# Kernel optimization log

Measured on AMD Instinct MI355X. Metric: run time of the kernel, lower is better.

Reference implementation:

```python
import jax, jax.numpy as jnp
import numpy as np

E = 1024  # embed_dim
R = 16    # LoRA rank
B = 4
S = 2048


def setup_inputs() -> dict:
    key = jax.random.key(0)
    ks = jax.random.split(key, 12)
    inp = {
        'query': jax.random.normal(ks[0], (B, S, E), jnp.float32),
        'key': jax.random.normal(ks[1], (B, S, E), jnp.float32),
        'value': jax.random.normal(ks[2], (B, S, E), jnp.float32),
        'Q_weight': jax.random.normal(ks[3], (E, E), jnp.float32) / np.sqrt(E),
        'K_weight': jax.random.normal(ks[4], (E, E), jnp.float32) / np.sqrt(E),
        'V_weight': jax.random.normal(ks[5], (E, E), jnp.float32) / np.sqrt(E),
        'Q_A': 0.02 * jax.random.normal(ks[6], (R, E), jnp.float32),
        'Q_B': 0.02 * jax.random.normal(ks[7], (E, R), jnp.float32),
        'K_A': 0.02 * jax.random.normal(ks[8], (R, E), jnp.float32),
        'K_B': 0.02 * jax.random.normal(ks[9], (E, R), jnp.float32),
        'V_A': 0.02 * jax.random.normal(ks[10], (R, E), jnp.float32),
        'V_B': 0.02 * jax.random.normal(ks[11], (E, R), jnp.float32),
        'O_weight': jax.random.normal(jax.random.fold_in(key, 99), (E, E), jnp.float32) / np.sqrt(E),
    }
    return inp


def reference(query, key, value, Q_weight, K_weight, V_weight,
              Q_A, Q_B, K_A, K_B, V_A, V_B, O_weight):
    embed_dim = Q_weight.shape[0]
    # base projections (linear(x, W) = x @ W.T) + low-rank LoRA deltas
    Q = jnp.einsum('bse,fe->bsf', query, Q_weight) + jnp.einsum('bse,re->bsr', query, Q_A) @ Q_B.T
    K = jnp.einsum('bse,fe->bsf', key, K_weight) + jnp.einsum('bse,re->bsr', key, K_A) @ K_B.T
    V = jnp.einsum('bse,fe->bsf', value, V_weight) + jnp.einsum('bse,re->bsr', value, V_A) @ V_B.T
    scores = jnp.einsum('bqe,bke->bqk', Q, K) / jnp.sqrt(jnp.float32(embed_dim))
    attn = jax.nn.softmax(scores, axis=-1)
    out = jnp.einsum('bqk,bke->bqe', attn, V)
    return jnp.einsum('bse,fe->bsf', out, O_weight)
```

## Files before the change

kernel.cpp:

```cpp
#include <hip/hip_runtime.h>


#define S_LEN 2048
#define E_DIM 1024

typedef __attribute__((ext_vector_type(8))) short short8;
typedef __attribute__((ext_vector_type(4))) float floatx4;

__device__ __forceinline__ unsigned short f2bf(float f) {
  union { float f; unsigned int u; } x; x.f = f;
  return (unsigned short)((x.u + 0x7fffu + ((x.u >> 16) & 1u)) >> 16);
}
__device__ __forceinline__ float bf2f(unsigned short h) {
  union { unsigned int u; float f; } x; x.u = ((unsigned int)h) << 16;
  return x.f;
}

__device__ __forceinline__ void gld_lds16(const unsigned short* g, unsigned short* l) {
  __builtin_amdgcn_global_load_lds(
      (const __attribute__((address_space(1))) unsigned int*)(const void*)g,
      (__attribute__((address_space(3))) unsigned int*)(void*)l,
      16, 0, 0);
}

template<bool LORA, bool OUTF32, bool OWNM>
__global__ __launch_bounds__(512, 2) void gemm256(
    const unsigned short* __restrict__ A, const unsigned short* __restrict__ B,
    void* __restrict__ Cv,
    const unsigned short* __restrict__ LA, const unsigned short* __restrict__ LB,
    long lda, long ldb, long ldc, int K, float scale,
    long batA, long batB, long batC, long batLA, long batLB) {
  __shared__ alignas(16) unsigned short As[2][2][8192];
  __shared__ alignas(16) unsigned short Bs[2][2][8192];

  const int tid  = threadIdx.x;
  const int wave = tid >> 6, lane = tid & 63;
  const int quad = lane >> 4, l16 = lane & 15;
  const int wr = wave >> 2, wc = wave & 3;
  const int bg = (wc & 1) * 4;

  const int Nx = (int)gridDim.x, Ny = (int)gridDim.y;
  const int wg2 = (int)blockIdx.x + Nx * (int)blockIdx.y;
  const int xcd = wg2 & 7, ii = wg2 >> 3;
  int bx, by;
  if constexpr (OWNM) {
    const int lg = 31 - __clz(Nx);
    by = xcd * (Ny >> 3) + (ii >> lg);
    bx = ii & (Nx - 1);
  } else {
    const int lg = 31 - __clz(Ny);
    bx = xcd * (Nx >> 3) + (ii >> lg);
    by = ii & (Ny - 1);
  }
  const long m0 = (long)by * 256;
  const long n0 = (long)bx * 256;
  const unsigned short* Az = A + (long)blockIdx.z * batA;
  const unsigned short* Bz = B + (long)blockIdx.z * batB;

  floatx4 acc[8][4];
#pragma unroll
  for (int i = 0; i < 8; ++i)
#pragma unroll
    for (int j = 0; j < 4; ++j) acc[i][j] = (floatx4){0.f, 0.f, 0.f, 0.f};

  const int c0r = ((tid >> 7) << 4) | (tid & 15);
  const int c0k = ((tid >> 4) & 7) << 3;
  const unsigned short* a0 = Az + (m0 + c0r) * lda + c0k;
  const unsigned short* b0 = Bz + (n0 + c0r) * ldb + c0k;

#define STG_A(bf, h, k0)                                                    \
  do {                                                                      \
    gld_lds16(a0 + (long)((h) * 128) * lda + (k0), &As[bf][h][tid * 8]);    \
    gld_lds16(a0 + (long)((h) * 128 + 64) * lda + (k0),                     \
              &As[bf][h][4096 + tid * 8]);                                  \
  } while (0)
#define STG_B(bf, h, k0)                                                    \
  do {                                                                      \
    gld_lds16(b0 + (long)((h) * 128) * ldb + (k0), &Bs[bf][h][tid * 8]);    \
    gld_lds16(b0 + (long)((h) * 128 + 64) * ldb + (k0),                     \
              &Bs[bf][h][4096 + tid * 8]);                                  \
  } while (0)

  STG_A(0, 0, 0); STG_A(0, 1, 0);
  STG_B(0, 0, 0); STG_B(0, 1, 0);
  STG_A(1, 0, 64); STG_A(1, 1, 64);

  const int NT = K >> 6;
#pragma unroll 2
  for (int t = 0; t < NT; ++t) {
    const int cur = t & 1;
    const int kB = (t + 1 < NT ? t + 1 : NT - 1) << 6;
    const int kA = (t + 2 < NT ? t + 2 : NT - 1) << 6;
    const unsigned short* ra = &As[cur][wr][0];
    const unsigned short* rb = &Bs[cur][wc >> 1][0];

    asm volatile("s_waitcnt vmcnt(4)\n\ts_barrier" ::: "memory");

    short8 a_[8][2], b_[4][2];
#pragma unroll
    for (int i = 0; i < 4; ++i)
#pragma unroll
      for (int ks = 0; ks < 2; ++ks)
        a_[i][ks] = *(const short8*)(ra + (i * 128 + ks * 64 + lane) * 8);
#pragma unroll
    for (int j = 0; j < 2; ++j)
#pragma unroll
      for (int ks = 0; ks < 2; ++ks)
        b_[j][ks] = *(const short8*)(rb + ((bg + j) * 128 + ks * 64 + lane) * 8);
    STG_B(cur ^ 1, 0, kB);
    asm volatile("s_barrier" ::: "memory");
    __builtin_amdgcn_s_setprio(1);
#pragma unroll
    for (int ks = 0; ks < 2; ++ks)
#pragma unroll
      for (int i = 0; i < 4; ++i)
#pragma unroll
        for (int j = 0; j < 2; ++j)
          acc[i][j] = __builtin_amdgcn_mfma_f32_16x16x32_bf16(a_[i][ks], b_[j][ks], acc[i][j], 0, 0, 0);
    __builtin_amdgcn_s_setprio(0);

#pragma unroll
    for (int i = 4; i < 8; ++i)
#pragma unroll
      for (int ks = 0; ks < 2; ++ks)
        a_[i][ks] = *(const short8*)(ra + (i * 128 + ks * 64 + lane) * 8);
#pragma unroll
    for (int j = 2; j < 4; ++j)
#pragma unroll
      for (int ks = 0; ks < 2; ++ks)
        b_[j][ks] = *(const short8*)(rb + ((bg + j) * 128 + ks * 64 + lane) * 8);
    STG_B(cur ^ 1, 1, kB);
    asm volatile("s_barrier" ::: "memory");
    __builtin_amdgcn_s_setprio(1);
#pragma unroll
    for (int ks = 0; ks < 2; ++ks)
#pragma unroll
      for (int i = 0; i < 4; ++i)
#pragma unroll
        for (int j = 2; j < 4; ++j)
          acc[i][j] = __builtin_amdgcn_mfma_f32_16x16x32_bf16(a_[i][ks], b_[j][ks], acc[i][j], 0, 0, 0);
    __builtin_amdgcn_s_setprio(0);
    asm volatile("s_waitcnt lgkmcnt(0)\n\ts_barrier" ::: "memory");

    STG_A(cur, 0, kA);
    __builtin_amdgcn_s_setprio(1);
#pragma unroll
    for (int ks = 0; ks < 2; ++ks)
#pragma unroll
      for (int i = 4; i < 8; ++i)
#pragma unroll
        for (int j = 0; j < 2; ++j)
          acc[i][j] = __builtin_amdgcn_mfma_f32_16x16x32_bf16(a_[i][ks], b_[j][ks], acc[i][j], 0, 0, 0);
    __builtin_amdgcn_s_setprio(0);

    STG_A(cur, 1, kA);
    __builtin_amdgcn_s_setprio(1);
#pragma unroll
    for (int ks = 0; ks < 2; ++ks)
#pragma unroll
      for (int i = 4; i < 8; ++i)
#pragma unroll
        for (int j = 2; j < 4; ++j)
          acc[i][j] = __builtin_amdgcn_mfma_f32_16x16x32_bf16(a_[i][ks], b_[j][ks], acc[i][j], 0, 0, 0);
    __builtin_amdgcn_s_setprio(0);
  }

  if constexpr (LORA) {
    __syncthreads();
    const unsigned short* LAz = LA + (long)blockIdx.z * batLA;
    const unsigned short* LBz = LB + (long)blockIdx.z * batLB;
#pragma unroll
    for (int cc = 0; cc < 4; ++cc) {
      const int c = cc * 512 + tid;
      const int h = c >> 10, ci = c & 1023;
      const int kc = (ci >> 4) & 7;
      const int row = h * 128 + ((ci >> 7) << 4) + (ci & 15);
      uint4 va, vb_;
      if (kc < 2) {
        va  = *(const uint4*)(LAz + (m0 + row) * 16 + kc * 8);
        vb_ = *(const uint4*)(LBz + (n0 + row) * 16 + kc * 8);
      } else {
        va.x = va.y = va.z = va.w = 0u; vb_ = va;
      }
      *(uint4*)(&As[0][h][ci * 8]) = va;
      *(uint4*)(&Bs[0][h][ci * 8]) = vb_;
    }
    __syncthreads();
    short8 a2[8], b2[4];
#pragma unroll
    for (int i = 0; i < 8; ++i)
      a2[i] = *(const short8*)(&As[0][wr][(i * 128 + lane) * 8]);
#pragma unroll
    for (int j = 0; j < 4; ++j)
      b2[j] = *(const short8*)(&Bs[0][wc >> 1][((bg + j) * 128 + lane) * 8]);
#pragma unroll
    for (int i = 0; i < 8; ++i)
#pragma unroll
      for (int j = 0; j < 4; ++j)
        acc[i][j] = __builtin_amdgcn_mfma_f32_16x16x32_bf16(a2[i], b2[j], acc[i][j], 0, 0, 0);
  } else {
    asm volatile("s_waitcnt vmcnt(0)" ::: "memory");
  }

#pragma unroll
  for (int i = 0; i < 8; ++i) {
    const long row = m0 + wr * 128 + i * 16 + quad * 4;
#pragma unroll
    for (int j = 0; j < 4; ++j) {
      const long col = n0 + wc * 64 + j * 16 + l16;
#pragma unroll
      for (int rr = 0; rr < 4; ++rr) {
        float val = acc[i][j][rr] * scale;
        if constexpr (OUTF32)
          ((float*)Cv)[(long)blockIdx.z * batC + (row + rr) * ldc + col] = val;
        else
          ((unsigned short*)Cv)[(long)blockIdx.z * batC + (row + rr) * ldc + col] = f2bf(val);
      }
    }
  }
#undef STG_A
#undef STG_B
}

__device__ __forceinline__ uint4 pack8(const float* x) {
  float4 a = *(const float4*)x;
  float4 b = *(const float4*)(x + 4);
  uint4 o;
  o.x = (unsigned int)f2bf(a.x) | ((unsigned int)f2bf(a.y) << 16);
  o.y = (unsigned int)f2bf(a.z) | ((unsigned int)f2bf(a.w) << 16);
  o.z = (unsigned int)f2bf(b.x) | ((unsigned int)f2bf(b.y) << 16);
  o.w = (unsigned int)f2bf(b.z) | ((unsigned int)f2bf(b.w) << 16);
  return o;
}

__global__ __launch_bounds__(256) void prep_qkv(
    const float* __restrict__ q, const float* __restrict__ k, const float* __restrict__ v,
    unsigned short* __restrict__ qb, unsigned short* __restrict__ kb,
    unsigned short* __restrict__ vb) {
  const float* X; unsigned short* Y;
  if (blockIdx.y == 0)      { X = q; Y = qb; }
  else if (blockIdx.y == 1) { X = k; Y = kb; }
  else                      { X = v; Y = vb; }
  const int tid = threadIdx.x;
  const long blk = (long)blockIdx.x * 16384;
#pragma unroll
  for (int it = 0; it < 8; ++it) {
    const long idx = blk + it * 2048 + tid * 8;
    *(uint4*)(Y + idx) = pack8(X + idx);
  }
}

__global__ __launch_bounds__(256) void cvt_all(
    const float* __restrict__ Wq, const float* __restrict__ Wk,
    const float* __restrict__ Wv, const float* __restrict__ Wo,
    const float* __restrict__ QB, const float* __restrict__ KB, const float* __restrict__ VB,
    const float* __restrict__ QA, const float* __restrict__ KA, const float* __restrict__ VA,
    unsigned short* __restrict__ wqb, unsigned short* __restrict__ wkb,
    unsigned short* __restrict__ wvb, unsigned short* __restrict__ wob,
    unsigned short* __restrict__ Bqb, unsigned short* __restrict__ Bkb, unsigned short* __restrict__ Bvb,
    unsigned short* __restrict__ Aqb, unsigned short* __restrict__ Akb, unsigned short* __restrict__ Avb) {
  if (blockIdx.y < 4) {
    const float* x; unsigned short* y;
    switch (blockIdx.y) {
      case 0: x = Wq; y = wqb; break;
      case 1: x = Wk; y = wkb; break;
      case 2: x = Wv; y = wvb; break;
      default: x = Wo; y = wob; break;
    }
    const long i = ((long)blockIdx.x * 256 + threadIdx.x) * 8;
    *(uint4*)(y + i) = pack8(x + i);
  } else {
    if (blockIdx.x >= 48) return;
    const int mat = blockIdx.x >> 3, sub = blockIdx.x & 7;
    const float* x; unsigned short* y;
    switch (mat) {
      case 0: x = QB; y = Bqb; break;
      case 1: x = KB; y = Bkb; break;
      case 2: x = VB; y = Bvb; break;
      case 3: x = QA; y = Aqb; break;
      case 4: x = KA; y = Akb; break;
      default: x = VA; y = Avb; break;
    }
    const long i = ((long)sub * 256 + threadIdx.x) * 8;
    *(uint4*)(y + i) = pack8(x + i);
  }
}

__global__ __launch_bounds__(256) void lora_t_mfma(
    const unsigned short* __restrict__ qb, const unsigned short* __restrict__ kb,
    const unsigned short* __restrict__ vb,
    const unsigned short* __restrict__ Aq, const unsigned short* __restrict__ Ak,
    const unsigned short* __restrict__ Av,
    unsigned short* __restrict__ Tq, unsigned short* __restrict__ Tk,
    unsigned short* __restrict__ Tv) {
  const unsigned short* X; const unsigned short* Am; unsigned short* T;
  if (blockIdx.y == 0)      { X = qb; Am = Aq; T = Tq; }
  else if (blockIdx.y == 1) { X = kb; Am = Ak; T = Tk; }
  else                      { X = vb; Am = Av; T = Tv; }
  const int tid = threadIdx.x, wave = tid >> 6, lane = tid & 63;
  const int quad = lane >> 4, l16 = lane & 15;
  const long m0 = (long)blockIdx.x * 64 + wave * 16;
  floatx4 acc = (floatx4){0.f, 0.f, 0.f, 0.f};
  const unsigned short* xp = X + (m0 + l16) * 1024 + quad * 8;
  const unsigned short* ap = Am + (long)l16 * 1024 + quad * 8;
#pragma unroll 4
  for (int k0 = 0; k0 < 1024; k0 += 32) {
    short8 af = *(const short8*)(xp + k0);
    short8 bf = *(const short8*)(ap + k0);
    acc = __builtin_amdgcn_mfma_f32_16x16x32_bf16(af, bf, acc, 0, 0, 0);
  }
#pragma unroll
  for (int rr = 0; rr < 4; ++rr)
    T[(m0 + quad * 4 + rr) * 16 + l16] = f2bf(acc[rr]);
}

__global__ __launch_bounds__(256) void softmax_kernel(unsigned short* __restrict__ S) {
  const long base = (long)blockIdx.x * 2048;
  const int tid = threadIdx.x;
  const int lane = tid & 63, wave = tid >> 6;
  __shared__ float redm[4], reds[4];
  uint4 raw = *(const uint4*)(S + base + tid * 8);
  unsigned int w[4] = {raw.x, raw.y, raw.z, raw.w};
  float v[8];
#pragma unroll
  for (int i = 0; i < 4; ++i) {
    v[2 * i]     = bf2f((unsigned short)(w[i] & 0xffffu));
    v[2 * i + 1] = bf2f((unsigned short)(w[i] >> 16));
  }
  float m = v[0];
#pragma unroll
  for (int i = 1; i < 8; ++i) m = fmaxf(m, v[i]);
  for (int off = 32; off >= 1; off >>= 1) m = fmaxf(m, __shfl_xor(m, off, 64));
  if (lane == 0) redm[wave] = m;
  __syncthreads();
  m = fmaxf(fmaxf(redm[0], redm[1]), fmaxf(redm[2], redm[3]));
  float e[8], s = 0.f;
#pragma unroll
  for (int i = 0; i < 8; ++i) { e[i] = __expf(v[i] - m); s += e[i]; }
  for (int off = 32; off >= 1; off >>= 1) s += __shfl_xor(s, off, 64);
  if (lane == 0) reds[wave] = s;
  __syncthreads();
  s = reds[0] + reds[1] + reds[2] + reds[3];
  const float inv = 1.0f / s;
  uint4 o;
  o.x = (unsigned int)f2bf(e[0] * inv) | ((unsigned int)f2bf(e[1] * inv) << 16);
  o.y = (unsigned int)f2bf(e[2] * inv) | ((unsigned int)f2bf(e[3] * inv) << 16);
  o.z = (unsigned int)f2bf(e[4] * inv) | ((unsigned int)f2bf(e[5] * inv) << 16);
  o.w = (unsigned int)f2bf(e[6] * inv) | ((unsigned int)f2bf(e[7] * inv) << 16);
  *(uint4*)(S + base + tid * 8) = o;
}

extern "C" void kernel_launch(void* const* d_in, const int* in_sizes, int n_in,
                              void* d_out, int out_size, void* d_ws, size_t ws_size,
                              hipStream_t stream) {
  const float* q  = (const float*)d_in[0];
  const float* k  = (const float*)d_in[1];
  const float* v  = (const float*)d_in[2];
  const float* Wq = (const float*)d_in[3];
  const float* Wk = (const float*)d_in[4];
  const float* Wv = (const float*)d_in[5];
  const float* QA = (const float*)d_in[6];
  const float* QB = (const float*)d_in[7];
  const float* KA = (const float*)d_in[8];
  const float* KB = (const float*)d_in[9];
  const float* VA = (const float*)d_in[10];
  const float* VB = (const float*)d_in[11];
  const float* Wo = (const float*)d_in[12];

  unsigned short* W = (unsigned short*)d_ws;
  const long SEe = (long)8192 * 1024;
  unsigned short* qb  = W;
  unsigned short* kb  = W + SEe;
  unsigned short* vb  = W + 2 * SEe;
  unsigned short* Qp  = W + 3 * SEe;
  unsigned short* Kp  = W + 4 * SEe;
  unsigned short* VT  = W + 5 * SEe;
  unsigned short* wqb = W + 6 * SEe;
  unsigned short* wkb = wqb + 1048576;
  unsigned short* wvb = wkb + 1048576;
  unsigned short* wob = wvb + 1048576;
  unsigned short* Bqb = wob + 1048576;
  unsigned short* Bkb = Bqb + 16384;
  unsigned short* Bvb = Bkb + 16384;
  unsigned short* Aqb = Bvb + 16384;
  unsigned short* Akb = Aqb + 16384;
  unsigned short* Avb = Akb + 16384;
  unsigned short* Tq  = Avb + 16384;
  unsigned short* Tk  = Tq + 131072;
  unsigned short* Tv  = Tk + 131072;
  unsigned short* scores = W;
  unsigned short* attn   = vb;

  dim3 blk(256, 1, 1), blk5(512, 1, 1);
  prep_qkv<<<dim3(512, 3, 1), blk, 0, stream>>>(q, k, v, qb, kb, vb);
  cvt_all<<<dim3(512, 5, 1), blk, 0, stream>>>(Wq, Wk, Wv, Wo, QB, KB, VB, QA, KA, VA,
                                               wqb, wkb, wvb, wob, Bqb, Bkb, Bvb, Aqb, Akb, Avb);
  lora_t_mfma<<<dim3(128, 3, 1), blk, 0, stream>>>(qb, kb, vb, Aqb, Akb, Avb, Tq, Tk, Tv);

  gemm256<true, false, true><<<dim3(4, 32, 2), blk5, 0, stream>>>(
      qb, wqb, Qp, Tq, Bqb, 1024, 1024, 1024, 1024, 1.0f,
      SEe, 1048576, SEe, 131072, 16384);
  gemm256<true, false, false><<<dim3(32, 4, 1), blk5, 0, stream>>>(
      wvb, vb, VT, Bvb, Tv, 1024, 1024, 8192, 1024, 1.0f, 0, 0, 0, 0, 0);
  gemm256<false, false, true><<<dim3(8, 8, 4), blk5, 0, stream>>>(
      Qp, Kp, scores, nullptr, nullptr, 1024, 1024, 2048, 1024, 0.03125f,
      (long)S_LEN * E_DIM, (long)S_LEN * E_DIM, (long)S_LEN * S_LEN, 0, 0);
  softmax_kernel<<<8192, blk, 0, stream>>>(scores);
  gemm256<false, false, true><<<dim3(4, 8, 4), blk5, 0, stream>>>(
      scores, VT, attn, nullptr, nullptr, 2048, 8192, 1024, 2048, 1.0f,
      (long)S_LEN * S_LEN, (long)S_LEN, (long)S_LEN * E_DIM, 0, 0);
  gemm256<false, true, true><<<dim3(4, 32, 1), blk5, 0, stream>>>(
      attn, wob, d_out, nullptr, nullptr, 1024, 1024, 1024, 1024, 1.0f, 0, 0, 0, 0, 0);
}
```

Baseline: 432.5 us.

## Template GEMM N-tile width and use 256x128 tiles for smaller GEMMs

Adds a BN template parameter so the GEMM can run with 256x128 output tiles, halving the B-tile LDS footprint and accumulator count, and uses it for the V projection, attn@V and output projection. This doubles block counts for those launches (128->256 or 256->512 blocks), filling more of the CUs. The main loop is also restructured to load per-k-step fragments (aLo/aHi, bb) with extra barriers instead of holding both k-substeps in registers, cutting register pressure but adding synchronisation and reducing A-tile reuse per block.

```diff
diff --git a/kernel.cpp b/kernel.cpp
--- a/kernel.cpp
+++ b/kernel.cpp
@@ -23,21 +23,24 @@
       16, 0, 0);
 }
 
-template<bool LORA, bool OUTF32, bool OWNM>
+template<bool LORA, bool OUTF32, bool OWNM, int BN>
 __global__ __launch_bounds__(512, 2) void gemm256(
     const unsigned short* __restrict__ A, const unsigned short* __restrict__ B,
     void* __restrict__ Cv,
     const unsigned short* __restrict__ LA, const unsigned short* __restrict__ LB,
     long lda, long ldb, long ldc, int K, float scale,
     long batA, long batB, long batC, long batLA, long batLB) {
+  constexpr int BNH = BN / 2;
+  constexpr int BCH = BNH * 8;
+  constexpr int JW  = BN / 64;
   __shared__ alignas(16) unsigned short As[2][2][8192];
-  __shared__ alignas(16) unsigned short Bs[2][2][8192];
+  __shared__ alignas(16) unsigned short Bs[2][2][BCH * 8];
 
   const int tid  = threadIdx.x;
   const int wave = tid >> 6, lane = tid & 63;
   const int quad = lane >> 4, l16 = lane & 15;
   const int wr = wave >> 2, wc = wave & 3;
-  const int bg = (wc & 1) * 4;
+  const int bg = (wc & 1) * JW;
 
   const int Nx = (int)gridDim.x, Ny = (int)gridDim.y;
   const int wg2 = (int)blockIdx.x + Nx * (int)blockIdx.y;
@@ -53,15 +56,15 @@
     by = ii & (Ny - 1);
   }
   const long m0 = (long)by * 256;
-  const long n0 = (long)bx * 256;
+  const long n0 = (long)bx * BN;
   const unsigned short* Az = A + (long)blockIdx.z * batA;
   const unsigned short* Bz = B + (long)blockIdx.z * batB;
 
-  floatx4 acc[8][4];
+  floatx4 acc[8][JW];
 #pragma unroll
   for (int i = 0; i < 8; ++i)
 #pragma unroll
-    for (int j = 0; j < 4; ++j) acc[i][j] = (floatx4){0.f, 0.f, 0.f, 0.f};
+    for (int j = 0; j < JW; ++j) acc[i][j] = (floatx4){0.f, 0.f, 0.f, 0.f};
 
   const int c0r = ((tid >> 7) << 4) | (tid & 15);
   const int c0k = ((tid >> 4) & 7) << 3;
@@ -76,9 +79,10 @@
   } while (0)
 #define STG_B(bf, h, k0)                                                    \
   do {                                                                      \
-    gld_lds16(b0 + (long)((h) * 128) * ldb + (k0), &Bs[bf][h][tid * 8]);    \
-    gld_lds16(b0 + (long)((h) * 128 + 64) * ldb + (k0),                     \
-              &Bs[bf][h][4096 + tid * 8]);                                  \
+    gld_lds16(b0 + (long)((h) * BNH) * ldb + (k0), &Bs[bf][h][tid * 8]);    \
+    if constexpr (BN == 256)                                                \
+      gld_lds16(b0 + (long)((h) * BNH + 64) * ldb + (k0),                   \
+                &Bs[bf][h][4096 + tid * 8]);                                \
   } while (0)
 
   STG_A(0, 0, 0); STG_A(0, 1, 0);
@@ -96,76 +100,73 @@
 
     asm volatile("s_waitcnt vmcnt(4)\n\ts_barrier" ::: "memory");
 
-    short8 a_[8][2], b_[4][2];
-#pragma unroll
-    for (int i = 0; i < 4; ++i)
-#pragma unroll
-      for (int ks = 0; ks < 2; ++ks)
-        a_[i][ks] = *(const short8*)(ra + (i * 128 + ks * 64 + lane) * 8);
-#pragma unroll
-    for (int j = 0; j < 2; ++j)
-#pragma unroll
-      for (int ks = 0; ks < 2; ++ks)
-        b_[j][ks] = *(const short8*)(rb + ((bg + j) * 128 + ks * 64 + lane) * 8);
+    short8 aLo[4], aHi[4], bb[JW];
+#pragma unroll
+    for (int i = 0; i < 4; ++i)
+      aLo[i] = *(const short8*)(ra + (i * 128 + lane) * 8);
+#pragma unroll
+    for (int j = 0; j < JW; ++j)
+      bb[j] = *(const short8*)(rb + ((bg + j) * 128 + lane) * 8);
     STG_B(cur ^ 1, 0, kB);
     asm volatile("s_barrier" ::: "memory");
     __builtin_amdgcn_s_setprio(1);
 #pragma unroll
-    for (int ks = 0; ks < 2; ++ks)
-#pragma unroll
-      for (int i = 0; i < 4; ++i)
-#pragma unroll
-        for (int j = 0; j < 2; ++j)
-          acc[i][j] = __builtin_amdgcn_mfma_f32_16x16x32_bf16(a_[i][ks], b_[j][ks], acc[i][j], 0, 0, 0);
+    for (int i = 0; i < 4; ++i)
+#pragma unroll
+      for (int j = 0; j < JW; ++j)
+        acc[i][j] = __builtin_amdgcn_mfma_f32_16x16x32_bf16(aLo[i], bb[j], acc[i][j], 0, 0, 0);
     __builtin_amdgcn_s_setprio(0);
-
-#pragma unroll
-    for (int i = 4; i < 8; ++i)
-#pragma unroll
-      for (int ks = 0; ks < 2; ++ks)
-        a_[i][ks] = *(const short8*)(ra + (i * 128 + ks * 64 + lane) * 8);
-#pragma unroll
-    for (int j = 2; j < 4; ++j)
-#pragma unroll
-      for (int ks = 0; ks < 2; ++ks)
-        b_[j][ks] = *(const short8*)(rb + ((bg + j) * 128 + ks * 64 + lane) * 8);
+    asm volatile("s_barrier" ::: "memory");
+
+#pragma unroll
+    for (int i = 0; i < 4; ++i)
+      aHi[i] = *(const short8*)(ra + ((i + 4) * 128 + lane) * 8);
     STG_B(cur ^ 1, 1, kB);
     asm volatile("s_barrier" ::: "memory");
     __builtin_amdgcn_s_setprio(1);
 #pragma unroll
-    for (int ks = 0; ks < 2; ++ks)
-#pragma unroll
-      for (int i = 0; i < 4; ++i)
-#pragma unroll
-        for (int j = 2; j < 4; ++j)
-          acc[i][j] = __builtin_amdgcn_mfma_f32_16x16x32_bf16(a_[i][ks], b_[j][ks], acc[i][j], 0, 0, 0);
+    for (int i = 0; i < 4; ++i)
+#pragma unroll
+      for (int j = 0; j < JW; ++j)
+        acc[i + 4][j] = __builtin_amdgcn_mfma_f32_16x16x32_bf16(aHi[i], bb[j], acc[i + 4][j], 0, 0, 0);
     __builtin_amdgcn_s_setprio(0);
+    asm volatile("s_barrier" ::: "memory");
+
+#pragma unroll
+    for (int i = 0; i < 4; ++i)
+      aLo[i] = *(const short8*)(ra + (i * 128 + 64 + lane) * 8);
+#pragma unroll
+    for (int j = 0; j < JW; ++j)
+      bb[j] = *(const short8*)(rb + ((bg + j) * 128 + 64 + lane) * 8);
+    asm volatile("s_barrier" ::: "memory");
+    __builtin_amdgcn_s_setprio(1);
+#pragma unroll
+    for (int i = 0; i < 4; ++i)
+#pragma unroll
+      for (int j = 0; j < JW; ++j)
+        acc[i][j] = __builtin_amdgcn_mfma_f32_16x16x32_bf16(aLo[i], bb[j], acc[i][j], 0, 0, 0);
+    __builtin_amdgcn_s_setprio(0);
+    asm volatile("s_barrier" ::: "memory");
+
+#pragma unroll
+    for (int i = 0; i < 4; ++i)
+      aHi[i] = *(const short8*)(ra + ((i + 4) * 128 + 64 + lane) * 8);
+    asm volatile("s_barrier" ::: "memory");
+    __builtin_amdgcn_s_setprio(1);
+#pragma unroll
+    for (int i = 0; i < 4; ++i)
+#pragma unroll
+      for (int j = 0; j < JW; ++j)
+        acc[i + 4][j] = __builtin_amdgcn_mfma_f32_16x16x32_bf16(aHi[i], bb[j], acc[i + 4][j], 0, 0, 0);
+    __builtin_amdgcn_s_setprio(0);
+
     asm volatile("s_waitcnt lgkmcnt(0)\n\ts_barrier" ::: "memory");
-
     STG_A(cur, 0, kA);
-    __builtin_amdgcn_s_setprio(1);
-#pragma unroll
-    for (int ks = 0; ks < 2; ++ks)
-#pragma unroll
-      for (int i = 4; i < 8; ++i)
-#pragma unroll
-        for (int j = 0; j < 2; ++j)
-          acc[i][j] = __builtin_amdgcn_mfma_f32_16x16x32_bf16(a_[i][ks], b_[j][ks], acc[i][j], 0, 0, 0);
-    __builtin_amdgcn_s_setprio(0);
-
     STG_A(cur, 1, kA);
-    __builtin_amdgcn_s_setprio(1);
-#pragma unroll
-    for (int ks = 0; ks < 2; ++ks)
-#pragma unroll
-      for (int i = 4; i < 8; ++i)
-#pragma unroll
-        for (int j = 2; j < 4; ++j)
-          acc[i][j] = __builtin_amdgcn_mfma_f32_16x16x32_bf16(a_[i][ks], b_[j][ks], acc[i][j], 0, 0, 0);
-    __builtin_amdgcn_s_setprio(0);
   }
 
   if constexpr (LORA) {
+    asm volatile("s_waitcnt vmcnt(0)" ::: "memory");
     __syncthreads();
     const unsigned short* LAz = LA + (long)blockIdx.z * batLA;
     const unsigned short* LBz = LB + (long)blockIdx.z * batLB;
@@ -175,28 +176,34 @@
       const int h = c >> 10, ci = c & 1023;
       const int kc = (ci >> 4) & 7;
       const int row = h * 128 + ((ci >> 7) << 4) + (ci & 15);
-      uint4 va, vb_;
-      if (kc < 2) {
-        va  = *(const uint4*)(LAz + (m0 + row) * 16 + kc * 8);
-        vb_ = *(const uint4*)(LBz + (n0 + row) * 16 + kc * 8);
-      } else {
-        va.x = va.y = va.z = va.w = 0u; vb_ = va;
-      }
+      uint4 va;
+      if (kc < 2) va = *(const uint4*)(LAz + (m0 + row) * 16 + kc * 8);
+      else { va.x = va.y = va.z = va.w = 0u; }
       *(uint4*)(&As[0][h][ci * 8]) = va;
+    }
+#pragma unroll
+    for (int cc = 0; cc < (2 * BCH) / 512; ++cc) {
+      const int c = cc * 512 + tid;
+      const int h = c / BCH, ci = c % BCH;
+      const int kc = (ci >> 4) & 7;
+      const int row = h * BNH + ((ci >> 7) << 4) + (ci & 15);
+      uint4 vb_;
+      if (kc < 2) vb_ = *(const uint4*)(LBz + (n0 + row) * 16 + kc * 8);
+      else { vb_.x = vb_.y = vb_.z = vb_.w = 0u; }
       *(uint4*)(&Bs[0][h][ci * 8]) = vb_;
     }
     __syncthreads();
-    short8 a2[8], b2[4];
+    short8 a2[8], b2[JW];
 #pragma unroll
     for (int i = 0; i < 8; ++i)
       a2[i] = *(const short8*)(&As[0][wr][(i * 128 + lane) * 8]);
 #pragma unroll
-    for (int j = 0; j < 4; ++j)
+    for (int j = 0; j < JW; ++j)
       b2[j] = *(const short8*)(&Bs[0][wc >> 1][((bg + j) * 128 + lane) * 8]);
 #pragma unroll
     for (int i = 0; i < 8; ++i)
 #pragma unroll
-      for (int j = 0; j < 4; ++j)
+      for (int j = 0; j < JW; ++j)
         acc[i][j] = __builtin_amdgcn_mfma_f32_16x16x32_bf16(a2[i], b2[j], acc[i][j], 0, 0, 0);
   } else {
     asm volatile("s_waitcnt vmcnt(0)" ::: "memory");
@@ -206,8 +213,8 @@
   for (int i = 0; i < 8; ++i) {
     const long row = m0 + wr * 128 + i * 16 + quad * 4;
 #pragma unroll
-    for (int j = 0; j < 4; ++j) {
-      const long col = n0 + wc * 64 + j * 16 + l16;
+    for (int j = 0; j < JW; ++j) {
+      const long col = n0 + wc * (16 * JW) + j * 16 + l16;
 #pragma unroll
       for (int rr = 0; rr < 4; ++rr) {
         float val = acc[i][j][rr] * scale;
@@ -397,18 +404,18 @@
                                                wqb, wkb, wvb, wob, Bqb, Bkb, Bvb, Aqb, Akb, Avb);
   lora_t_mfma<<<dim3(128, 3, 1), blk, 0, stream>>>(qb, kb, vb, Aqb, Akb, Avb, Tq, Tk, Tv);
 
-  gemm256<true, false, true><<<dim3(4, 32, 2), blk5, 0, stream>>>(
+  gemm256<true, false, true, 256><<<dim3(4, 32, 2), blk5, 0, stream>>>(
       qb, wqb, Qp, Tq, Bqb, 1024, 1024, 1024, 1024, 1.0f,
       SEe, 1048576, SEe, 131072, 16384);
-  gemm256<true, false, false><<<dim3(32, 4, 1), blk5, 0, stream>>>(
+  gemm256<true, false, false, 128><<<dim3(64, 4, 1), blk5, 0, stream>>>(
       wvb, vb, VT, Bvb, Tv, 1024, 1024, 8192, 1024, 1.0f, 0, 0, 0, 0, 0);
-  gemm256<false, false, true><<<dim3(8, 8, 4), blk5, 0, stream>>>(
+  gemm256<false, false, true, 256><<<dim3(8, 8, 4), blk5, 0, stream>>>(
       Qp, Kp, scores, nullptr, nullptr, 1024, 1024, 2048, 1024, 0.03125f,
       (long)S_LEN * E_DIM, (long)S_LEN * E_DIM, (long)S_LEN * S_LEN, 0, 0);
   softmax_kernel<<<8192, blk, 0, stream>>>(scores);
-  gemm256<false, false, true><<<dim3(4, 8, 4), blk5, 0, stream>>>(
+  gemm256<false, false, true, 128><<<dim3(8, 8, 4), blk5, 0, stream>>>(
       scores, VT, attn, nullptr, nullptr, 2048, 8192, 1024, 2048, 1.0f,
       (long)S_LEN * S_LEN, (long)S_LEN, (long)S_LEN * E_DIM, 0, 0);
-  gemm256<false, true, true><<<dim3(4, 32, 1), blk5, 0, stream>>>(
+  gemm256<false, true, true, 128><<<dim3(8, 32, 1), blk5, 0, stream>>>(
       attn, wob, d_out, nullptr, nullptr, 1024, 1024, 1024, 1024, 1.0f, 0, 0, 0, 0, 0);
 }
```

Result: slower. 461.1 us (+6.6%).

## Restructure GEMM into eight-phase pipeline with XOR-swizzled LDS layout

Applied to the files above, without the earlier changes.

Rewrites the main GEMM loop as four quadrant phases. Each phase loads only the A/B fragments it needs and issues the next tile's global-to-LDS copy for one half of A or B. LDS staging uses an XOR swizzle on row-major 64-wide K tiles to avoid bank conflicts, and the LoRA epilogue now reads the rank-16 factors straight from global memory instead of staging them through LDS with extra syncthreads. The aim is better overlap of loads with MFMA work and fewer LDS conflicts, at the cost of more barriers per iteration and a more delicate wait-count schedule.

```diff
diff --git a/kernel.cpp b/kernel.cpp
--- a/kernel.cpp
+++ b/kernel.cpp
@@ -24,7 +24,7 @@
 }
 
 template<bool LORA, bool OUTF32, bool OWNM>
-__global__ __launch_bounds__(512, 2) void gemm256(
+__global__ __launch_bounds__(512, 2) void gemm8p(
     const unsigned short* __restrict__ A, const unsigned short* __restrict__ B,
     void* __restrict__ Cv,
     const unsigned short* __restrict__ LA, const unsigned short* __restrict__ LB,
@@ -37,7 +37,6 @@
   const int wave = tid >> 6, lane = tid & 63;
   const int quad = lane >> 4, l16 = lane & 15;
   const int wr = wave >> 2, wc = wave & 3;
-  const int bg = (wc & 1) * 4;
 
   const int Nx = (int)gridDim.x, Ny = (int)gridDim.y;
   const int wg2 = (int)blockIdx.x + Nx * (int)blockIdx.y;
@@ -63,52 +62,51 @@
 #pragma unroll
     for (int j = 0; j < 4; ++j) acc[i][j] = (floatx4){0.f, 0.f, 0.f, 0.f};
 
-  const int c0r = ((tid >> 7) << 4) | (tid & 15);
-  const int c0k = ((tid >> 4) & 7) << 3;
-  const unsigned short* a0 = Az + (m0 + c0r) * lda + c0k;
-  const unsigned short* b0 = Bz + (n0 + c0r) * ldb + c0k;
-
-#define STG_A(bf, h, k0)                                                    \
-  do {                                                                      \
-    gld_lds16(a0 + (long)((h) * 128) * lda + (k0), &As[bf][h][tid * 8]);    \
-    gld_lds16(a0 + (long)((h) * 128 + 64) * lda + (k0),                     \
-              &As[bf][h][4096 + tid * 8]);                                  \
+  const int lr = tid >> 3;
+  const int sp = (tid & 7) ^ (lr & 7);
+  const unsigned short* aS = Az + (m0 + lr) * lda + sp * 8;
+  const unsigned short* bS = Bz + (n0 + (lr >> 5) * 64 + (lr & 31)) * ldb + sp * 8;
+
+#define STG_A(bf, F, k0)                                                     \
+  do {                                                                       \
+    gld_lds16(aS + (long)((F) * 64) * lda + (k0), &As[bf][F][tid * 8]);      \
+    gld_lds16(aS + (long)((F) * 64 + 128) * lda + (k0),                      \
+              &As[bf][F][4096 + tid * 8]);                                   \
   } while (0)
-#define STG_B(bf, h, k0)                                                    \
-  do {                                                                      \
-    gld_lds16(b0 + (long)((h) * 128) * ldb + (k0), &Bs[bf][h][tid * 8]);    \
-    gld_lds16(b0 + (long)((h) * 128 + 64) * ldb + (k0),                     \
-              &Bs[bf][h][4096 + tid * 8]);                                  \
+#define STG_B(bf, G, k0)                                                     \
+  do {                                                                       \
+    gld_lds16(bS + (long)((G) * 32) * ldb + (k0), &Bs[bf][G][tid * 8]);      \
+    gld_lds16(bS + (long)((G) * 32 + 128) * ldb + (k0),                      \
+              &Bs[bf][G][4096 + tid * 8]);                                   \
   } while (0)
 
-  STG_A(0, 0, 0); STG_A(0, 1, 0);
-  STG_B(0, 0, 0); STG_B(0, 1, 0);
-  STG_A(1, 0, 64); STG_A(1, 1, 64);
+  const int xo    = (l16 & 7) << 4;
+  const int aoff0 = ((quad * 16) ^ xo) >> 1;
+  const int aoff1 = ((64 + quad * 16) ^ xo) >> 1;
+  const int arow  = wr * 4096 + l16 * 64;
+  const int brow  = wc * 2048 + l16 * 64;
+
+  STG_A(0, 0, 0); STG_B(0, 0, 0); STG_A(0, 1, 0); STG_B(0, 1, 0);
 
   const int NT = K >> 6;
-#pragma unroll 2
   for (int t = 0; t < NT; ++t) {
-    const int cur = t & 1;
-    const int kB = (t + 1 < NT ? t + 1 : NT - 1) << 6;
-    const int kA = (t + 2 < NT ? t + 2 : NT - 1) << 6;
-    const unsigned short* ra = &As[cur][wr][0];
-    const unsigned short* rb = &Bs[cur][wc >> 1][0];
+    const int cur = t & 1, nbf = cur ^ 1;
+    const int kN = (t + 1 < NT ? t + 1 : NT - 1) << 6;
+    short8 aLo[4][2], aHi[4][2], b0f[2][2], b1f[2][2];
 
     asm volatile("s_waitcnt vmcnt(4)\n\ts_barrier" ::: "memory");
-
-    short8 a_[8][2], b_[4][2];
-#pragma unroll
-    for (int i = 0; i < 4; ++i)
-#pragma unroll
-      for (int ks = 0; ks < 2; ++ks)
-        a_[i][ks] = *(const short8*)(ra + (i * 128 + ks * 64 + lane) * 8);
-#pragma unroll
-    for (int j = 0; j < 2; ++j)
-#pragma unroll
-      for (int ks = 0; ks < 2; ++ks)
-        b_[j][ks] = *(const short8*)(rb + ((bg + j) * 128 + ks * 64 + lane) * 8);
-    STG_B(cur ^ 1, 0, kB);
-    asm volatile("s_barrier" ::: "memory");
+#pragma unroll
+    for (int i = 0; i < 4; ++i) {
+      aLo[i][0] = *(const short8*)&As[cur][0][arow + i * 1024 + aoff0];
+      aLo[i][1] = *(const short8*)&As[cur][0][arow + i * 1024 + aoff1];
+    }
+#pragma unroll
+    for (int j = 0; j < 2; ++j) {
+      b0f[j][0] = *(const short8*)&Bs[cur][0][brow + j * 1024 + aoff0];
+      b0f[j][1] = *(const short8*)&Bs[cur][0][brow + j * 1024 + aoff1];
+    }
+    STG_A(nbf, 0, kN);
+    asm volatile("s_waitcnt lgkmcnt(0)" ::: "memory");
     __builtin_amdgcn_s_setprio(1);
 #pragma unroll
     for (int ks = 0; ks < 2; ++ks)
@@ -116,90 +114,83 @@
       for (int i = 0; i < 4; ++i)
 #pragma unroll
         for (int j = 0; j < 2; ++j)
-          acc[i][j] = __builtin_amdgcn_mfma_f32_16x16x32_bf16(a_[i][ks], b_[j][ks], acc[i][j], 0, 0, 0);
+          acc[i][j] = __builtin_amdgcn_mfma_f32_16x16x32_bf16(
+              aLo[i][ks], b0f[j][ks], acc[i][j], 0, 0, 0);
     __builtin_amdgcn_s_setprio(0);
 
-#pragma unroll
-    for (int i = 4; i < 8; ++i)
-#pragma unroll
-      for (int ks = 0; ks < 2; ++ks)
-        a_[i][ks] = *(const short8*)(ra + (i * 128 + ks * 64 + lane) * 8);
-#pragma unroll
-    for (int j = 2; j < 4; ++j)
-#pragma unroll
-      for (int ks = 0; ks < 2; ++ks)
-        b_[j][ks] = *(const short8*)(rb + ((bg + j) * 128 + ks * 64 + lane) * 8);
-    STG_B(cur ^ 1, 1, kB);
-    asm volatile("s_barrier" ::: "memory");
+    asm volatile("s_waitcnt vmcnt(4)\n\ts_barrier" ::: "memory");
+#pragma unroll
+    for (int i = 0; i < 4; ++i) {
+      aHi[i][0] = *(const short8*)&As[cur][1][arow + i * 1024 + aoff0];
+      aHi[i][1] = *(const short8*)&As[cur][1][arow + i * 1024 + aoff1];
+    }
+    STG_B(nbf, 0, kN);
+    asm volatile("s_waitcnt lgkmcnt(0)" ::: "memory");
     __builtin_amdgcn_s_setprio(1);
 #pragma unroll
     for (int ks = 0; ks < 2; ++ks)
 #pragma unroll
       for (int i = 0; i < 4; ++i)
 #pragma unroll
-        for (int j = 2; j < 4; ++j)
-          acc[i][j] = __builtin_amdgcn_mfma_f32_16x16x32_bf16(a_[i][ks], b_[j][ks], acc[i][j], 0, 0, 0);
+        for (int j = 0; j < 2; ++j)
+          acc[i + 4][j] = __builtin_amdgcn_mfma_f32_16x16x32_bf16(
+              aHi[i][ks], b0f[j][ks], acc[i + 4][j], 0, 0, 0);
     __builtin_amdgcn_s_setprio(0);
-    asm volatile("s_waitcnt lgkmcnt(0)\n\ts_barrier" ::: "memory");
-
-    STG_A(cur, 0, kA);
+
+    asm volatile("s_waitcnt vmcnt(4)\n\ts_barrier" ::: "memory");
+#pragma unroll
+    for (int j = 0; j < 2; ++j) {
+      b1f[j][0] = *(const short8*)&Bs[cur][1][brow + j * 1024 + aoff0];
+      b1f[j][1] = *(const short8*)&Bs[cur][1][brow + j * 1024 + aoff1];
+    }
+    STG_A(nbf, 1, kN);
+    asm volatile("s_waitcnt lgkmcnt(0)" ::: "memory");
     __builtin_amdgcn_s_setprio(1);
 #pragma unroll
     for (int ks = 0; ks < 2; ++ks)
 #pragma unroll
-      for (int i = 4; i < 8; ++i)
+      for (int i = 0; i < 4; ++i)
 #pragma unroll
         for (int j = 0; j < 2; ++j)
-          acc[i][j] = __builtin_amdgcn_mfma_f32_16x16x32_bf16(a_[i][ks], b_[j][ks], acc[i][j], 0, 0, 0);
+          acc[i][j + 2] = __builtin_amdgcn_mfma_f32_16x16x32_bf16(
+              aLo[i][ks], b1f[j][ks], acc[i][j + 2], 0, 0, 0);
     __builtin_amdgcn_s_setprio(0);
 
-    STG_A(cur, 1, kA);
+    __builtin_amdgcn_s_barrier();
+    STG_B(nbf, 1, kN);
     __builtin_amdgcn_s_setprio(1);
 #pragma unroll
     for (int ks = 0; ks < 2; ++ks)
 #pragma unroll
-      for (int i = 4; i < 8; ++i)
-#pragma unroll
-        for (int j = 2; j < 4; ++j)
-          acc[i][j] = __builtin_amdgcn_mfma_f32_16x16x32_bf16(a_[i][ks], b_[j][ks], acc[i][j], 0, 0, 0);
+      for (int i = 0; i < 4; ++i)
+#pragma unroll
+        for (int j = 0; j < 2; ++j)
+          acc[i + 4][j + 2] = __builtin_amdgcn_mfma_f32_16x16x32_bf16(
+              aHi[i][ks], b1f[j][ks], acc[i + 4][j + 2], 0, 0, 0);
     __builtin_amdgcn_s_setprio(0);
   }
 
+  asm volatile("s_waitcnt vmcnt(0)" ::: "memory");
+
   if constexpr (LORA) {
-    __syncthreads();
     const unsigned short* LAz = LA + (long)blockIdx.z * batLA;
     const unsigned short* LBz = LB + (long)blockIdx.z * batLB;
-#pragma unroll
-    for (int cc = 0; cc < 4; ++cc) {
-      const int c = cc * 512 + tid;
-      const int h = c >> 10, ci = c & 1023;
-      const int kc = (ci >> 4) & 7;
-      const int row = h * 128 + ((ci >> 7) << 4) + (ci & 15);
-      uint4 va, vb_;
-      if (kc < 2) {
-        va  = *(const uint4*)(LAz + (m0 + row) * 16 + kc * 8);
-        vb_ = *(const uint4*)(LBz + (n0 + row) * 16 + kc * 8);
-      } else {
-        va.x = va.y = va.z = va.w = 0u; vb_ = va;
-      }
-      *(uint4*)(&As[0][h][ci * 8]) = va;
-      *(uint4*)(&Bs[0][h][ci * 8]) = vb_;
-    }
-    __syncthreads();
-    short8 a2[8], b2[4];
-#pragma unroll
-    for (int i = 0; i < 8; ++i)
-      a2[i] = *(const short8*)(&As[0][wr][(i * 128 + lane) * 8]);
-#pragma unroll
-    for (int j = 0; j < 4; ++j)
-      b2[j] = *(const short8*)(&Bs[0][wc >> 1][((bg + j) * 128 + lane) * 8]);
-#pragma unroll
-    for (int i = 0; i < 8; ++i)
+    const short8 z8 = {0, 0, 0, 0, 0, 0, 0, 0};
+    short8 b2[4];
+#pragma unroll
+    for (int j = 0; j < 4; ++j) {
+      const long row = n0 + wc * 64 + j * 16 + l16;
+      b2[j] = (quad < 2) ? *(const short8*)(LBz + row * 16 + quad * 8) : z8;
+    }
+#pragma unroll
+    for (int i = 0; i < 8; ++i) {
+      const long row = m0 + wr * 128 + i * 16 + l16;
+      const short8 a2 =
+          (quad < 2) ? *(const short8*)(LAz + row * 16 + quad * 8) : z8;
 #pragma unroll
       for (int j = 0; j < 4; ++j)
-        acc[i][j] = __builtin_amdgcn_mfma_f32_16x16x32_bf16(a2[i], b2[j], acc[i][j], 0, 0, 0);
-  } else {
-    asm volatile("s_waitcnt vmcnt(0)" ::: "memory");
+        acc[i][j] = __builtin_amdgcn_mfma_f32_16x16x32_bf16(a2, b2[j], acc[i][j], 0, 0, 0);
+    }
   }
 
 #pragma unroll
@@ -397,18 +388,18 @@
                                                wqb, wkb, wvb, wob, Bqb, Bkb, Bvb, Aqb, Akb, Avb);
   lora_t_mfma<<<dim3(128, 3, 1), blk, 0, stream>>>(qb, kb, vb, Aqb, Akb, Avb, Tq, Tk, Tv);
 
-  gemm256<true, false, true><<<dim3(4, 32, 2), blk5, 0, stream>>>(
+  gemm8p<true, false, true><<<dim3(4, 32, 2), blk5, 0, stream>>>(
       qb, wqb, Qp, Tq, Bqb, 1024, 1024, 1024, 1024, 1.0f,
       SEe, 1048576, SEe, 131072, 16384);
-  gemm256<true, false, false><<<dim3(32, 4, 1), blk5, 0, stream>>>(
+  gemm8p<true, false, false><<<dim3(32, 4, 1), blk5, 0, stream>>>(
       wvb, vb, VT, Bvb, Tv, 1024, 1024, 8192, 1024, 1.0f, 0, 0, 0, 0, 0);
-  gemm256<false, false, true><<<dim3(8, 8, 4), blk5, 0, stream>>>(
+  gemm8p<false, false, true><<<dim3(8, 8, 4), blk5, 0, stream>>>(
       Qp, Kp, scores, nullptr, nullptr, 1024, 1024, 2048, 1024, 0.03125f,
       (long)S_LEN * E_DIM, (long)S_LEN * E_DIM, (long)S_LEN * S_LEN, 0, 0);
   softmax_kernel<<<8192, blk, 0, stream>>>(scores);
-  gemm256<false, false, true><<<dim3(4, 8, 4), blk5, 0, stream>>>(
+  gemm8p<false, false, true><<<dim3(4, 8, 4), blk5, 0, stream>>>(
       scores, VT, attn, nullptr, nullptr, 2048, 8192, 1024, 2048, 1.0f,
       (long)S_LEN * S_LEN, (long)S_LEN, (long)S_LEN * E_DIM, 0, 0);
-  gemm256<false, true, true><<<dim3(4, 32, 1), blk5, 0, stream>>>(
+  gemm8p<false, true, true><<<dim3(4, 32, 1), blk5, 0, stream>>>(
       attn, wob, d_out, nullptr, nullptr, 1024, 1024, 1024, 1024, 1.0f, 0, 0, 0, 0, 0);
 }
```

After: 380.3 us. 1.14x faster.
